# Kernel optimization log

Hardware: AMD Instinct MI355X
Metric: run time of the kernel (lower is better)

Reference implementation:

```python
import jax, jax.numpy as jnp
import numpy as np

BETA = 0.9
THRESHOLD = 1.0
ATAN_ALPHA = 2.0  # snntorch default surrogate.atan() alpha


@jax.custom_vjp
def spike_fn(x):
    # Heaviside step with ATan surrogate gradient (snntorch default)
    return (x > 0).astype(x.dtype)


def _spike_fwd(x):
    return spike_fn(x), x


def _spike_bwd(x, g):
    grad = g * (ATAN_ALPHA / 2.0) / (1.0 + (jnp.pi / 2.0 * ATAN_ALPHA * x) ** 2)
    return (grad,)


spike_fn.defvjp(_spike_fwd, _spike_bwd)


def setup_inputs() -> dict:
    key = jax.random.key(0)
    k1, k2, k3 = jax.random.split(key, 3)
    batch, seq, input_dim, hidden, actions = 256, 128, 512, 2048, 512
    x = jax.random.normal(k1, (batch, seq, input_dim), dtype=jnp.float32)
    # kaiming_uniform_(a=0.01): bound = sqrt(6 / ((1 + a^2) * fan_in))
    b1_bound = float(np.sqrt(6.0 / ((1 + 0.01 ** 2) * input_dim)))
    b2_bound = float(np.sqrt(6.0 / ((1 + 0.01 ** 2) * hidden)))
    W1 = jax.random.uniform(k2, (hidden, input_dim), jnp.float32, -b1_bound, b1_bound)
    W2 = jax.random.uniform(k3, (actions, hidden), jnp.float32, -b2_bound, b2_bound)
    b1 = jnp.zeros((hidden,), jnp.float32)
    b2 = jnp.zeros((actions,), jnp.float32)
    return {"x": x, "W1": W1, "b1": b1, "W2": W2, "b2": b2}


def reference(x, W1, b1, W2, b2):
    # x: [batch, seq, input_dim]
    batch = x.shape[0]
    hidden = W1.shape[0]
    # precompute all fc1 currents at once (parallel over time)
    cur = jnp.einsum('bsi,hi->sbh', x, W1) + b1  # [seq, batch, hidden]

    def step(mem, cur_t):
        # snntorch Leaky, reset_mechanism='subtract':
        # reset computed from previous mem, detached
        reset = jax.lax.stop_gradient((mem > THRESHOLD).astype(mem.dtype))
        mem_new = BETA * mem + cur_t - reset * THRESHOLD
        spk = spike_fn(mem_new - THRESHOLD)
        return mem_new, spk

    mem0 = jnp.zeros((batch, hidden), dtype=x.dtype)
    _, spks = jax.lax.scan(step, mem0, cur)  # spks: [seq, batch, hidden]
    out = jnp.einsum('sbh,ah->bsa', spks, W2) + b2  # [batch, seq, actions]
    return out
```

## Files before the change

### kernel.cpp

```cpp
#include <hip/hip_runtime.h>

typedef __attribute__((ext_vector_type(8))) short short8;
typedef __attribute__((ext_vector_type(4))) float f32x4;

__device__ __forceinline__ unsigned short f2bf(float f) {
    unsigned int u = __float_as_uint(f);
    unsigned int r = (u + 0x7FFFu + ((u >> 16) & 1u)) >> 16;
    return (unsigned short)r;
}

__device__ __forceinline__ void gload16(const void* g, void* l) {
    __builtin_amdgcn_global_load_lds(
        (const __attribute__((address_space(1))) unsigned int*)g,
        (__attribute__((address_space(3))) unsigned int*)l,
        16, 0, 0);
}

__global__ __launch_bounds__(256) void k_tw(const float* __restrict__ W1,
                                            float* __restrict__ W1Tt) {
    const int tx = threadIdx.x & 31, ty = threadIdx.x >> 5;
    const int k0 = blockIdx.x * 32, j0 = blockIdx.y * 32, hc = blockIdx.z;
    __shared__ float t[32][33];
#pragma unroll
    for (int i = 0; i < 4; ++i)
        t[ty + i * 8][tx] = W1[(size_t)(hc * 128 + j0 + ty + i * 8) * 512 + k0 + tx];
    __syncthreads();
#pragma unroll
    for (int i = 0; i < 4; ++i)
        W1Tt[(size_t)hc * 65536 + (size_t)(k0 + ty + i * 8) * 128 + j0 + tx] =
            t[tx][ty + i * 8];
}

__global__ __launch_bounds__(256) void k_fc1_scan(
    const float* __restrict__ x,
    const float* __restrict__ W1Tt,
    const float* __restrict__ b1,
    unsigned short* __restrict__ spk)
{
    const int hc  = blockIdx.x;
    const int b   = blockIdx.y;
    const int tid = threadIdx.x;
    const int tx  = tid & 15;
    const int ty  = tid >> 4;

    __shared__ float lds[12288];

    const float* xb   = x    + (size_t)b * 65536;
    const float* wt   = W1Tt + (size_t)(hc >> 1) * 65536;
    const int    hoff = (hc & 1) * 64;

    float  acc[8][4]  = {};
    double accd[8][4] = {};

    auto stage = [&](int p, int k0) {
        float* Ab = lds + p * 6144;
        float* Bb = lds + p * 6144 + 4096;
#pragma unroll
        for (int it = 0; it < 4; ++it) {
            int t = tid + it * 256;
            int row = t >> 3, g = t & 7;
            gload16(xb + (size_t)row * 512 + k0 + ((g ^ ((row >> 3) & 7)) << 2),
                    Ab + t * 4);
        }
#pragma unroll
        for (int it = 0; it < 2; ++it) {
            int t2 = tid + it * 256;
            int kk2 = t2 >> 4, c = (t2 & 15) << 2;
            gload16(wt + (size_t)(k0 + kk2) * 128 + hoff + c, Bb + t2 * 4);
        }
    };

    auto compute = [&](int p) {
        const float* Ab = lds + p * 6144;
        const float* Bb = lds + p * 6144 + 4096;
#pragma unroll
        for (int k4 = 0; k4 < 8; ++k4) {
            float4 av[8];
#pragma unroll
            for (int i = 0; i < 8; ++i)
                av[i] = *(const float4*)(Ab + (ty * 8 + i) * 32 +
                                         ((k4 ^ (ty & 7)) << 2));
#pragma unroll
            for (int kk = 0; kk < 4; ++kk) {
                const float4 c0 = *(const float4*)(Bb + (k4 * 4 + kk) * 64 + tx * 4);
#pragma unroll
                for (int i = 0; i < 8; ++i) {
                    const float a = (kk == 0) ? av[i].x : (kk == 1) ? av[i].y
                                  : (kk == 2) ? av[i].z : av[i].w;
                    acc[i][0] = fmaf(a, c0.x, acc[i][0]);
                    acc[i][1] = fmaf(a, c0.y, acc[i][1]);
                    acc[i][2] = fmaf(a, c0.z, acc[i][2]);
                    acc[i][3] = fmaf(a, c0.w, acc[i][3]);
                }
            }
        }
    };

    stage(0, 0);
    __syncthreads();
    for (int kt = 0; kt < 16; ++kt) {
        if (kt < 15) stage((kt + 1) & 1, (kt + 1) * 32);
        compute(kt & 1);
#pragma unroll
        for (int i = 0; i < 8; ++i)
#pragma unroll
            for (int j = 0; j < 4; ++j) {
                accd[i][j] += (double)acc[i][j];
                acc[i][j] = 0.f;
            }
        __syncthreads();
    }

#pragma unroll
    for (int i = 0; i < 8; ++i) {
        const int r = ty * 8 + i;
        float4 v;
        v.x = (float)accd[i][0]; v.y = (float)accd[i][1];
        v.z = (float)accd[i][2]; v.w = (float)accd[i][3];
        *(float4*)(lds + r * 72 + tx * 4) = v;
    }
    __syncthreads();

    if (tid < 64) {
        const float b1v = b1[hc * 64 + tid];
        double mem = 0.0;
        size_t base = ((size_t)b * 128) * 2048 + (size_t)hc * 64 + tid;
        for (int s = 0; s < 128; ++s) {
            float curf = lds[s * 72 + tid] + b1v;
            double reset = (mem > 1.0) ? 1.0 : 0.0;
            mem = 0.9 * mem + (double)curf - reset;
            spk[base + (size_t)s * 2048] = (mem > 1.0) ? (unsigned short)0x3F80u
                                                       : (unsigned short)0u;
        }
    }
}

__global__ __launch_bounds__(256) void k_cvt(const float* __restrict__ W2,
                                             unsigned short* __restrict__ W2b)
{
    int i = blockIdx.x * 256 + threadIdx.x;
    float4 v = ((const float4*)W2)[i];
    ushort4 o;
    o.x = f2bf(v.x); o.y = f2bf(v.y); o.z = f2bf(v.z); o.w = f2bf(v.w);
    ((ushort4*)W2b)[i] = o;
}

__global__ __launch_bounds__(256) void k_fc2(
    const unsigned short* __restrict__ A,
    const unsigned short* __restrict__ B,
    const float* __restrict__ b2,
    float* __restrict__ out)
{
    __shared__ char ldsb[16384];
    char* As = ldsb;
    char* Bs = ldsb + 8192;

    const int tid  = threadIdx.x;
    const int m0   = blockIdx.y * 128;
    const int n0   = blockIdx.x * 128;
    const int lane = tid & 63;
    const int wv   = tid >> 6;
    const int wm   = wv >> 1, wn = wv & 1;
    const int lr   = lane & 15;
    const int lk   = lane >> 4;

    f32x4 acc[4][4] = {};

    const char* gA = (const char*)(A + (size_t)m0 * 2048);
    const char* gB = (const char*)(B + (size_t)n0 * 2048);

    for (int kt = 0; kt < 64; ++kt) {
        const int kb = kt * 64;
        __syncthreads();
#pragma unroll
        for (int inst = 0; inst < 2; ++inst) {
            int o   = tid * 16 + inst * 4096;
            int row = o >> 6;
            int cb  = o & 63;
            gload16(gA + (size_t)row * 4096 + kb + cb, As + o);
            gload16(gB + (size_t)row * 4096 + kb + cb, Bs + o);
        }
        __syncthreads();

        short8 af[4], bf[4];
#pragma unroll
        for (int mi = 0; mi < 4; ++mi)
            af[mi] = *(const short8*)(As + (wm * 64 + mi * 16 + lr) * 64 + lk * 16);
#pragma unroll
        for (int ni = 0; ni < 4; ++ni)
            bf[ni] = *(const short8*)(Bs + (wn * 64 + ni * 16 + lr) * 64 + lk * 16);
#pragma unroll
        for (int mi = 0; mi < 4; ++mi)
#pragma unroll
            for (int ni = 0; ni < 4; ++ni)
                acc[mi][ni] = __builtin_amdgcn_mfma_f32_16x16x32_bf16(
                    af[mi], bf[ni], acc[mi][ni], 0, 0, 0);
    }

    float b2v[4];
#pragma unroll
    for (int ni = 0; ni < 4; ++ni) b2v[ni] = b2[n0 + wn * 64 + ni * 16 + lr];

#pragma unroll
    for (int mi = 0; mi < 4; ++mi) {
        const int rb = m0 + wm * 64 + mi * 16 + lk * 4;
#pragma unroll
        for (int ni = 0; ni < 4; ++ni) {
            const int c = n0 + wn * 64 + ni * 16 + lr;
#pragma unroll
            for (int r = 0; r < 4; ++r)
                out[(size_t)(rb + r) * 512 + c] = acc[mi][ni][r] + b2v[ni];
        }
    }
}

extern "C" void kernel_launch(void* const* d_in, const int* in_sizes, int n_in,
                              void* d_out, int out_size, void* d_ws, size_t ws_size,
                              hipStream_t stream) {
    const float* x  = (const float*)d_in[0];
    const float* W1 = (const float*)d_in[1];
    const float* b1 = (const float*)d_in[2];
    const float* W2 = (const float*)d_in[3];
    const float* b2 = (const float*)d_in[4];
    float* out = (float*)d_out;

    unsigned short* spk  = (unsigned short*)d_ws;
    unsigned short* W2b  = (unsigned short*)((char*)d_ws + 134217728);
    float*          W1Tt = (float*)((char*)d_ws + 136314880);

    k_tw      <<<dim3(16, 4, 16), 256, 0, stream>>>(W1, W1Tt);
    k_fc1_scan<<<dim3(32, 256),   256, 0, stream>>>(x, W1Tt, b1, spk);
    k_cvt     <<<dim3(1024),      256, 0, stream>>>(W2, W2b);
    k_fc2     <<<dim3(4, 256),    256, 0, stream>>>(spk, W2b, b2, out);
}
```

Baseline: 1.130 ms.

## Read fc1 A operand directly from global and use packed FMA

The x tile is no longer staged through LDS. Each thread now loads its eight A rows straight from global memory (relying on cache broadcast across the 16 threads that share a row), and only the W1 tile stays double-buffered in shared memory. The inner FMA loop is rewritten with two-wide float vectors so the compiler can emit packed fp32 FMA instructions. This cuts LDS traffic and footprint, but adds global-memory latency inside the compute loop with no prefetching.

```diff
diff --git a/kernel.cpp b/kernel.cpp
--- a/kernel.cpp
+++ b/kernel.cpp
@@ -2,6 +2,16 @@
 
 typedef __attribute__((ext_vector_type(8))) short short8;
 typedef __attribute__((ext_vector_type(4))) float f32x4;
+typedef __attribute__((ext_vector_type(2))) float f32x2;
+
+#if __has_builtin(__builtin_elementwise_fma)
+#define PKFMA(a, b, c) __builtin_elementwise_fma(a, b, c)
+#else
+static __device__ __forceinline__ f32x2 PKFMA(f32x2 a, f32x2 b, f32x2 c) {
+    f32x2 d; d[0] = fmaf(a[0], b[0], c[0]); d[1] = fmaf(a[1], b[1], c[1]);
+    return d;
+}
+#endif
 
 __device__ __forceinline__ unsigned short f2bf(float f) {
     unsigned int u = __float_as_uint(f);
@@ -43,25 +53,18 @@
     const int tx  = tid & 15;
     const int ty  = tid >> 4;
 
-    __shared__ float lds[12288];
+    __shared__ float lds[9216];
 
     const float* xb   = x    + (size_t)b * 65536;
     const float* wt   = W1Tt + (size_t)(hc >> 1) * 65536;
     const int    hoff = (hc & 1) * 64;
-
-    float  acc[8][4]  = {};
+    const float* arow = xb + (size_t)(ty * 8) * 512;
+
+    f32x2  acc2[8][2] = {};
     double accd[8][4] = {};
 
-    auto stage = [&](int p, int k0) {
-        float* Ab = lds + p * 6144;
-        float* Bb = lds + p * 6144 + 4096;
-#pragma unroll
-        for (int it = 0; it < 4; ++it) {
-            int t = tid + it * 256;
-            int row = t >> 3, g = t & 7;
-            gload16(xb + (size_t)row * 512 + k0 + ((g ^ ((row >> 3) & 7)) << 2),
-                    Ab + t * 4);
-        }
+    auto stageB = [&](int p, int k0) {
+        float* Bb = lds + p * 2048;
 #pragma unroll
         for (int it = 0; it < 2; ++it) {
             int t2 = tid + it * 256;
@@ -70,44 +73,44 @@
         }
     };
 
-    auto compute = [&](int p) {
-        const float* Ab = lds + p * 6144;
-        const float* Bb = lds + p * 6144 + 4096;
+    auto computeTile = [&](int p, int k0) {
+        const float* Bb = lds + p * 2048;
 #pragma unroll
         for (int k4 = 0; k4 < 8; ++k4) {
             float4 av[8];
 #pragma unroll
             for (int i = 0; i < 8; ++i)
-                av[i] = *(const float4*)(Ab + (ty * 8 + i) * 32 +
-                                         ((k4 ^ (ty & 7)) << 2));
+                av[i] = *(const float4*)(arow + (size_t)i * 512 + k0 + k4 * 4);
 #pragma unroll
             for (int kk = 0; kk < 4; ++kk) {
                 const float4 c0 = *(const float4*)(Bb + (k4 * 4 + kk) * 64 + tx * 4);
+                f32x2 b01, b23;
+                b01[0] = c0.x; b01[1] = c0.y;
+                b23[0] = c0.z; b23[1] = c0.w;
 #pragma unroll
                 for (int i = 0; i < 8; ++i) {
                     const float a = (kk == 0) ? av[i].x : (kk == 1) ? av[i].y
                                   : (kk == 2) ? av[i].z : av[i].w;
-                    acc[i][0] = fmaf(a, c0.x, acc[i][0]);
-                    acc[i][1] = fmaf(a, c0.y, acc[i][1]);
-                    acc[i][2] = fmaf(a, c0.z, acc[i][2]);
-                    acc[i][3] = fmaf(a, c0.w, acc[i][3]);
+                    f32x2 aa; aa[0] = a; aa[1] = a;
+                    acc2[i][0] = PKFMA(aa, b01, acc2[i][0]);
+                    acc2[i][1] = PKFMA(aa, b23, acc2[i][1]);
                 }
             }
         }
     };
 
-    stage(0, 0);
+    stageB(0, 0);
     __syncthreads();
     for (int kt = 0; kt < 16; ++kt) {
-        if (kt < 15) stage((kt + 1) & 1, (kt + 1) * 32);
-        compute(kt & 1);
-#pragma unroll
-        for (int i = 0; i < 8; ++i)
-#pragma unroll
-            for (int j = 0; j < 4; ++j) {
-                accd[i][j] += (double)acc[i][j];
-                acc[i][j] = 0.f;
-            }
+        if (kt < 15) stageB((kt + 1) & 1, (kt + 1) * 32);
+        computeTile(kt & 1, kt * 32);
+#pragma unroll
+        for (int i = 0; i < 8; ++i) {
+            accd[i][0] += (double)acc2[i][0][0]; acc2[i][0][0] = 0.f;
+            accd[i][1] += (double)acc2[i][0][1]; acc2[i][0][1] = 0.f;
+            accd[i][2] += (double)acc2[i][1][0]; acc2[i][1][0] = 0.f;
+            accd[i][3] += (double)acc2[i][1][1]; acc2[i][1][1] = 0.f;
+        }
         __syncthreads();
     }
 
```

New measurement: 1.367 ms. 21.0% more time.
